# Kernel optimization log

Measured on AMD Instinct MI355X. Metric: run time of the kernel, lower is better.

Reference implementation:

```python
import jax, jax.numpy as jnp
import numpy as np

BN_EPS = 1e-5

def setup_inputs() -> dict:
    key = jax.random.key(0)
    ks = jax.random.split(key, 12)
    B = 32768
    x = jax.random.normal(ks[0], (B, 1, 28, 28), dtype=jnp.float32)
    conv_w = jax.random.normal(ks[1], (5, 1, 6, 6), dtype=jnp.float32) * 0.1
    conv_b = jax.random.normal(ks[2], (5,), dtype=jnp.float32) * 0.1
    bn2_gamma = jnp.ones((5,), jnp.float32) + jax.random.normal(ks[3], (5,), jnp.float32) * 0.05
    bn2_beta = jax.random.normal(ks[4], (5,), jnp.float32) * 0.05
    bn2_mean = jax.random.normal(ks[5], (5,), jnp.float32) * 0.1
    bn2_var = jax.random.uniform(ks[6], (5,), jnp.float32, 0.5, 1.5)
    fc_w = jax.random.normal(ks[7], (10, 125), dtype=jnp.float32) * 0.1
    fc_b = jax.random.normal(ks[8], (10,), dtype=jnp.float32) * 0.1
    bn1_gamma = jnp.ones((10,), jnp.float32) + jax.random.normal(ks[9], (10,), jnp.float32) * 0.05
    bn1_beta = jax.random.normal(ks[10], (10,), jnp.float32) * 0.05
    bn1_mean = jax.random.normal(ks[11], (10,), jnp.float32) * 0.1
    bn1_var = jnp.ones((10,), jnp.float32)
    return {"x": x, "conv_w": conv_w, "conv_b": conv_b,
            "bn2_gamma": bn2_gamma, "bn2_beta": bn2_beta, "bn2_mean": bn2_mean, "bn2_var": bn2_var,
            "fc_w": fc_w, "fc_b": fc_b,
            "bn1_gamma": bn1_gamma, "bn1_beta": bn1_beta, "bn1_mean": bn1_mean, "bn1_var": bn1_var}

def _sign(t):
    # torch Binarize = tensor.sign()
    return jnp.sign(t)

def reference(x, conv_w, conv_b, bn2_gamma, bn2_beta, bn2_mean, bn2_var,
              fc_w, fc_b, bn1_gamma, bn1_beta, bn1_mean, bn1_var):
    # BinarizeConv2d: binarize both input (C_in=1 != 3) and weight
    xb = _sign(x)
    wb = _sign(conv_w)
    y = jax.lax.conv_general_dilated(
        xb, wb, window_strides=(6, 6), padding=((2, 2), (2, 2)),
        dimension_numbers=("NCHW", "OIHW", "NCHW"))  # [B,5,5,5]
    y = y + conv_b[None, :, None, None]
    # BatchNorm2d (eval-mode running stats)
    y = (y - bn2_mean[None, :, None, None]) * (bn2_gamma / jnp.sqrt(bn2_var + BN_EPS))[None, :, None, None] + bn2_beta[None, :, None, None]
    # Hardtanh
    y = jnp.clip(y, -1.0, 1.0)
    # flatten to [B, 125]
    y = y.reshape(-1, 125)
    # BinarizeLinear: binarize input (125 != 784) and weight
    z = _sign(y) @ _sign(fc_w).T + fc_b
    # BatchNorm1d
    z = (z - bn1_mean) * (bn1_gamma / jnp.sqrt(bn1_var + BN_EPS)) + bn1_beta
    return jax.nn.log_softmax(z, axis=1)
```

## Files before the change

kernel.cpp:

```cpp
#include <hip/hip_runtime.h>
#include <cstdint>

#define BLK 256
#define SPB 16
#define HDRW 16
#define WPS 196
#define XS_INTS (HDRW + SPB*WPS)
#define YS_W 33
#define NQ 12
#define NREM (SPB*WPS - NQ*BLK)

#define W0_OFF  0
#define W1P_OFF 30
#define FC_OFF  45
#define CSC_OFF 375
#define CBI_OFF 380
#define FSC_OFF 385
#define FBI_OFF 395
#define WS_TOT  405

#if defined(__has_builtin)
# if __has_builtin(__builtin_amdgcn_sdot4)
#  define HAVE_SDOT4 1
# endif
#endif

__device__ __forceinline__ int dot4i8(int a, int b, int c) {
#ifdef HAVE_SDOT4
    return __builtin_amdgcn_sdot4(a, b, c, false);
#else
    int r = c;
    r += (((int)(a << 24)) >> 24) * (((int)(b << 24)) >> 24);
    r += (((int)(a << 16)) >> 24) * (((int)(b << 16)) >> 24);
    r += (((int)(a <<  8)) >> 24) * (((int)(b <<  8)) >> 24);
    r += (a >> 24) * (b >> 24);
    return r;
#endif
}

__device__ __forceinline__ int pack_sign4(float4 v) {
    int b0 = (v.x > 0.f) - (v.x < 0.f);
    int b1 = (v.y > 0.f) - (v.y < 0.f);
    int b2 = (v.z > 0.f) - (v.z < 0.f);
    int b3 = (v.w > 0.f) - (v.w < 0.f);
    return (b0 & 0xFF) | ((b1 & 0xFF) << 8) | ((b2 & 0xFF) << 16) | (b3 << 24);
}

__device__ __forceinline__ int sign8(float f) { return (f > 0.f) - (f < 0.f); }

__global__ __launch_bounds__(BLK, 2)
void bnn_fused(const float* __restrict__ x,
               const float* __restrict__ conv_w, const float* __restrict__ conv_b,
               const float* __restrict__ bn2_g,  const float* __restrict__ bn2_b,
               const float* __restrict__ bn2_m,  const float* __restrict__ bn2_v,
               const float* __restrict__ fc_w,   const float* __restrict__ fc_b,
               const float* __restrict__ bn1_g,  const float* __restrict__ bn1_b,
               const float* __restrict__ bn1_m,  const float* __restrict__ bn1_v,
               float* __restrict__ out)
{
    __shared__ int   xsi[XS_INTS];
    __shared__ int   ysi[SPB * YS_W];
    __shared__ int   wsS[WS_TOT];
    __shared__ float zf[SPB * 10];

    const int tid = threadIdx.x;
    const int blk = blockIdx.x;

    const float4* xg = (const float4*)x + (size_t)blk * (SPB * WPS);
    float4 v[NQ]; float4 vr;
    #pragma unroll
    for (int k = 0; k < NQ; k++) v[k] = xg[tid + k * BLK];
    const bool hasr = tid < NREM;
    if (hasr) vr = xg[tid + NQ * BLK];

    if (tid < 30) {
        int c = tid / 6, kr = tid - c * 6;
        const float* wp = conv_w + c * 36 + kr * 6;
        uint32_t a = 0;
        #pragma unroll
        for (int k = 0; k < 4; k++) a |= (uint32_t)(sign8(wp[k]) & 0xFF) << (8 * k);
        wsS[W0_OFF + tid] = (int)a;
    } else if (tid >= 32 && tid < 47) {
        int i = tid - 32, c = i / 3, p = i - c * 3;
        const float* wp = conv_w + c * 36;
        uint32_t a = 0;
        a |= (uint32_t)(sign8(wp[(2*p)*6 + 4]) & 0xFF);
        a |= (uint32_t)(sign8(wp[(2*p)*6 + 5]) & 0xFF) << 8;
        a |= (uint32_t)(sign8(wp[(2*p+1)*6 + 4]) & 0xFF) << 16;
        a |= (uint32_t)(sign8(wp[(2*p+1)*6 + 5]) & 0xFF) << 24;
        wsS[W1P_OFF + i] = (int)a;
    } else if (tid >= 48 && tid < 53) {
        int c = tid - 48;
        float sc = bn2_g[c] / sqrtf(bn2_v[c] + 1e-5f);
        wsS[CSC_OFF + c] = __float_as_int(sc);
        wsS[CBI_OFF + c] = __float_as_int((conv_b[c] - bn2_m[c]) * sc + bn2_b[c]);
    } else if (tid >= 64 && tid < 74) {
        int o = tid - 64;
        float sc = bn1_g[o] / sqrtf(bn1_v[o] + 1e-5f);
        wsS[FSC_OFF + o] = __float_as_int(sc);
        wsS[FBI_OFF + o] = __float_as_int((fc_b[o] - bn1_m[o]) * sc + bn1_b[o]);
    }
    for (int i = tid; i < 330; i += BLK) {
        int o = i / 33, w = i - o * 33;
        uint32_t m = 0;
        #pragma unroll
        for (int k = 0; k < 4; k++) {
            int kk = w * 4 + k;
            if (kk < 125) m |= (uint32_t)(sign8(fc_w[o * 125 + kk]) & 0xFF) << (8 * k);
        }
        wsS[FC_OFF + i] = (int)m;
    }

    if (tid < HDRW) xsi[tid] = 0;
    for (int i = tid; i < SPB * YS_W; i += BLK) ysi[i] = 0;

    #pragma unroll
    for (int k = 0; k < NQ; k++) xsi[HDRW + tid + k * BLK] = pack_sign4(v[k]);
    if (hasr) xsi[HDRW + tid + NQ * BLK] = pack_sign4(vr);
    __syncthreads();

    {
        int w0[30], w1p[15]; float csc[5], cbi[5];
        #pragma unroll
        for (int i = 0; i < 30; i++) w0[i]  = wsS[W0_OFF + i];
        #pragma unroll
        for (int i = 0; i < 15; i++) w1p[i] = wsS[W1P_OFF + i];
        #pragma unroll
        for (int c = 0; c < 5; c++) {
            csc[c] = __int_as_float(wsS[CSC_OFF + c]);
            cbi[c] = __int_as_float(wsS[CBI_OFF + c]);
        }
        #pragma unroll
        for (int it = 0; it < 2; it++) {
            int j = tid + it * BLK;
            if (j < SPB * 25) {
                int s  = j / 25, pos = j - s * 25;
                int oh = pos / 5, ow  = pos - oh * 5;
                int rowb = s * 784 + 168 * oh + 6 * ow - 58;
                int q  = (64 + rowb) >> 2;
                int sh = (rowb & 3) * 8;
                uint32_t emask = (ow == 0) ? 0xFFFF0000u : 0xFFFFFFFFu;
                uint32_t e0[6], e1[6];
                #pragma unroll
                for (int kr = 0; kr < 6; kr++) {
                    int a = q + 7 * kr;
                    if (kr < 2) a = (oh == 0) ? 0 : a;
                    uint32_t a0 = (uint32_t)xsi[a];
                    uint32_t a1 = (uint32_t)xsi[a + 1];
                    uint64_t vv = ((((uint64_t)a1) << 32) | a0) >> sh;
                    e0[kr] = (uint32_t)vv & emask;
                    e1[kr] = (uint32_t)(vv >> 32) & 0xFFFFu;
                }
                uint32_t e1p[3];
                #pragma unroll
                for (int p = 0; p < 3; p++) e1p[p] = e1[2*p] | (e1[2*p+1] << 16);
                #pragma unroll
                for (int c = 0; c < 5; c++) {
                    int acc = 0;
                    #pragma unroll
                    for (int kr = 0; kr < 6; kr++) acc = dot4i8((int)e0[kr], w0[c*6+kr], acc);
                    #pragma unroll
                    for (int p = 0; p < 3; p++)    acc = dot4i8((int)e1p[p], w1p[c*3+p], acc);
                    float yv = (float)acc * csc[c] + cbi[c];
                    ((signed char*)ysi)[s * (YS_W*4) + c * 25 + pos] = (signed char)sign8(yv);
                }
            }
        }
    }
    __syncthreads();

    if (tid < SPB * 10) {
        int s = tid / 10, o = tid - s * 10;
        int acc = 0;
        #pragma unroll
        for (int w = 0; w < 32; w++)
            acc = dot4i8(ysi[s * YS_W + w], wsS[FC_OFF + o * 33 + w], acc);
        zf[tid] = (float)acc * __int_as_float(wsS[FSC_OFF + o])
                             + __int_as_float(wsS[FBI_OFF + o]);
    }
    __syncthreads();

    if (tid < SPB) {
        float vv[10], mx = -1e30f;
        #pragma unroll
        for (int o = 0; o < 10; o++) { vv[o] = zf[tid * 10 + o]; mx = fmaxf(mx, vv[o]); }
        float l = 0.f;
        #pragma unroll
        for (int o = 0; o < 10; o++) l += __expf(vv[o] - mx);
        float lse = mx + __logf(l);
        #pragma unroll
        for (int o = 0; o < 10; o++) zf[tid * 10 + o] = vv[o] - lse;
    }
    __syncthreads();

    for (int i = tid; i < SPB * 10; i += BLK)
        out[(size_t)blk * (SPB * 10) + i] = zf[i];
}

extern "C" void kernel_launch(void* const* d_in, const int* in_sizes, int n_in,
                              void* d_out, int out_size, void* d_ws, size_t ws_size,
                              hipStream_t stream)
{
    const float* xp     = (const float*)d_in[0];
    const float* conv_w = (const float*)d_in[1];
    const float* conv_b = (const float*)d_in[2];
    const float* bn2_g  = (const float*)d_in[3];
    const float* bn2_b  = (const float*)d_in[4];
    const float* bn2_m  = (const float*)d_in[5];
    const float* bn2_v  = (const float*)d_in[6];
    const float* fc_w   = (const float*)d_in[7];
    const float* fc_b   = (const float*)d_in[8];
    const float* bn1_g  = (const float*)d_in[9];
    const float* bn1_b  = (const float*)d_in[10];
    const float* bn1_m  = (const float*)d_in[11];
    const float* bn1_v  = (const float*)d_in[12];
    float* outp = (float*)d_out;

    const int B = in_sizes[0] / 784;
    const int grid = B / SPB;
    bnn_fused<<<grid, BLK, 0, stream>>>(xp, conv_w, conv_b,
                                        bn2_g, bn2_b, bn2_m, bn2_v,
                                        fc_w, fc_b, bn1_g, bn1_b, bn1_m, bn1_v,
                                        outp);
}
```

Measured before the change: 178.2 us.

## Make each wave own its samples and drop block barriers after staging

Each of the four waves now loads, sign-packs, convolves and classifies its own 4-sample slab in shared memory. This removes the three block-wide barriers that followed the conv stage. The FC stage maps 16 lanes per sample and computes log-softmax with in-register width-16 shuffle reductions, so the zf shared buffer and the serial per-sample softmax thread are gone. Output is written straight from lanes. Launch bounds are raised to 4 blocks per CU, which adds register pressure and relies on wave-level ordering of shared-memory accesses without explicit fences.

```diff
diff --git a/kernel.cpp b/kernel.cpp
--- a/kernel.cpp
+++ b/kernel.cpp
@@ -2,13 +2,15 @@
 #include <cstdint>
 
 #define BLK 256
-#define SPB 16
+#define WAVES 4
+#define SPW 4
+#define SPB (WAVES*SPW)
+#define WPS 196
 #define HDRW 16
-#define WPS 196
-#define XS_INTS (HDRW + SPB*WPS)
+#define SLAB (SPW*WPS)
+#define XS_INTS (HDRW + WAVES*SLAB)
 #define YS_W 33
-#define NQ 12
-#define NREM (SPB*WPS - NQ*BLK)
+#define YSLAB (SPW*YS_W)
 
 #define W0_OFF  0
 #define W1P_OFF 30
@@ -48,7 +50,7 @@
 
 __device__ __forceinline__ int sign8(float f) { return (f > 0.f) - (f < 0.f); }
 
-__global__ __launch_bounds__(BLK, 2)
+__global__ __launch_bounds__(BLK, 4)
 void bnn_fused(const float* __restrict__ x,
                const float* __restrict__ conv_w, const float* __restrict__ conv_b,
                const float* __restrict__ bn2_g,  const float* __restrict__ bn2_b,
@@ -58,20 +60,21 @@
                const float* __restrict__ bn1_m,  const float* __restrict__ bn1_v,
                float* __restrict__ out)
 {
-    __shared__ int   xsi[XS_INTS];
-    __shared__ int   ysi[SPB * YS_W];
-    __shared__ int   wsS[WS_TOT];
-    __shared__ float zf[SPB * 10];
-
-    const int tid = threadIdx.x;
-    const int blk = blockIdx.x;
-
-    const float4* xg = (const float4*)x + (size_t)blk * (SPB * WPS);
-    float4 v[NQ]; float4 vr;
+    __shared__ int xsi[XS_INTS];
+    __shared__ int ysi[WAVES * YSLAB];
+    __shared__ int wsS[WS_TOT];
+
+    const int tid  = threadIdx.x;
+    const int lane = tid & 63;
+    const int wid  = tid >> 6;
+    const int blk  = blockIdx.x;
+
+    const float4* xg = (const float4*)x + ((size_t)blk * SPB + wid * SPW) * WPS;
+    float4 v[12]; float4 vr;
     #pragma unroll
-    for (int k = 0; k < NQ; k++) v[k] = xg[tid + k * BLK];
-    const bool hasr = tid < NREM;
-    if (hasr) vr = xg[tid + NQ * BLK];
+    for (int k = 0; k < 12; k++) v[k] = xg[lane + k * 64];
+    const bool hasr = lane < (SLAB - 12 * 64);
+    if (hasr) vr = xg[lane + 12 * 64];
 
     if (tid < 30) {
         int c = tid / 6, kr = tid - c * 6;
@@ -110,14 +113,18 @@
         }
         wsS[FC_OFF + i] = (int)m;
     }
-
     if (tid < HDRW) xsi[tid] = 0;
-    for (int i = tid; i < SPB * YS_W; i += BLK) ysi[i] = 0;
-
+
+    __syncthreads();
+
+    ysi[wid * YSLAB + lane]      = 0;
+    ysi[wid * YSLAB + lane + 64] = 0;
+    if (lane < YSLAB - 128) ysi[wid * YSLAB + 128 + lane] = 0;
+
+    int* xsw = xsi + HDRW + wid * SLAB;
     #pragma unroll
-    for (int k = 0; k < NQ; k++) xsi[HDRW + tid + k * BLK] = pack_sign4(v[k]);
-    if (hasr) xsi[HDRW + tid + NQ * BLK] = pack_sign4(vr);
-    __syncthreads();
+    for (int k = 0; k < 12; k++) xsw[lane + k * 64] = pack_sign4(v[k]);
+    if (hasr) xsw[lane + 12 * 64] = pack_sign4(vr);
 
     {
         int w0[30], w1p[15]; float csc[5], cbi[5];
@@ -132,11 +139,12 @@
         }
         #pragma unroll
         for (int it = 0; it < 2; it++) {
-            int j = tid + it * BLK;
-            if (j < SPB * 25) {
-                int s  = j / 25, pos = j - s * 25;
+            int jw = lane + it * 64;
+            if (jw < SPW * 25) {
+                int sl = jw / 25, pos = jw - sl * 25;
+                int ss = wid * SPW + sl;
                 int oh = pos / 5, ow  = pos - oh * 5;
-                int rowb = s * 784 + 168 * oh + 6 * ow - 58;
+                int rowb = ss * 784 + 168 * oh + 6 * ow - 58;
                 int q  = (64 + rowb) >> 2;
                 int sh = (rowb & 3) * 8;
                 uint32_t emask = (ow == 0) ? 0xFFFF0000u : 0xFFFFFFFFu;
@@ -162,39 +170,35 @@
                     #pragma unroll
                     for (int p = 0; p < 3; p++)    acc = dot4i8((int)e1p[p], w1p[c*3+p], acc);
                     float yv = (float)acc * csc[c] + cbi[c];
-                    ((signed char*)ysi)[s * (YS_W*4) + c * 25 + pos] = (signed char)sign8(yv);
+                    ((signed char*)ysi)[(ss * YS_W) * 4 + c * 25 + pos] = (signed char)sign8(yv);
                 }
             }
         }
     }
-    __syncthreads();
-
-    if (tid < SPB * 10) {
-        int s = tid / 10, o = tid - s * 10;
+
+    {
+        int sl = lane >> 4;
+        int oo = lane & 15;
+        int ss = wid * SPW + sl;
+        int oc = (oo < 10) ? oo : 0;
         int acc = 0;
         #pragma unroll
         for (int w = 0; w < 32; w++)
-            acc = dot4i8(ysi[s * YS_W + w], wsS[FC_OFF + o * 33 + w], acc);
-        zf[tid] = (float)acc * __int_as_float(wsS[FSC_OFF + o])
-                             + __int_as_float(wsS[FBI_OFF + o]);
-    }
-    __syncthreads();
-
-    if (tid < SPB) {
-        float vv[10], mx = -1e30f;
-        #pragma unroll
-        for (int o = 0; o < 10; o++) { vv[o] = zf[tid * 10 + o]; mx = fmaxf(mx, vv[o]); }
-        float l = 0.f;
-        #pragma unroll
-        for (int o = 0; o < 10; o++) l += __expf(vv[o] - mx);
-        float lse = mx + __logf(l);
-        #pragma unroll
-        for (int o = 0; o < 10; o++) zf[tid * 10 + o] = vv[o] - lse;
-    }
-    __syncthreads();
-
-    for (int i = tid; i < SPB * 10; i += BLK)
-        out[(size_t)blk * (SPB * 10) + i] = zf[i];
+            acc = dot4i8(ysi[ss * YS_W + w], wsS[FC_OFF + oc * 33 + w], acc);
+        float z = (oo < 10)
+            ? (float)acc * __int_as_float(wsS[FSC_OFF + oc]) + __int_as_float(wsS[FBI_OFF + oc])
+            : -1e30f;
+        float mx = z;
+        #pragma unroll
+        for (int m = 1; m < 16; m <<= 1) mx = fmaxf(mx, __shfl_xor(mx, m, 16));
+        float e = (oo < 10) ? __expf(z - mx) : 0.f;
+        float sum = e;
+        #pragma unroll
+        for (int m = 1; m < 16; m <<= 1) sum += __shfl_xor(sum, m, 16);
+        float res = z - mx - __logf(sum);
+        if (oo < 10)
+            out[((size_t)blk * SPB + ss) * 10 + oo] = res;
+    }
 }
 
 extern "C" void kernel_launch(void* const* d_in, const int* in_sizes, int n_in,
```

Result: no change. 178.2 us (+0.0%).
